# Kernel tuning notes

Measured on AMD Instinct MI355X. Metric: run time of the kernel, lower is better.

## Reference

```python
import jax, jax.numpy as jnp
import numpy as np

B, N, F, R, H = 128, 196, 2048, 1024, 512

def setup_inputs() -> dict:
    key = jax.random.key(0)
    ks = jax.random.split(key, 16)
    u = lambda k, shape, s=0.1: jax.random.uniform(k, shape, jnp.float32, -s, s)
    inp = {
        'att_seq': jax.random.normal(ks[0], (B, N, F), jnp.float32),
        'mil_feats': jax.random.normal(ks[1], (B, 1000), jnp.float32),
        'matching_feats': jax.random.normal(ks[2], (B, 1000), jnp.float32),
        'h': jax.random.normal(ks[3], (B, R), jnp.float32),
        'c': jax.random.normal(ks[4], (B, R), jnp.float32),
        # params (torch Linear convention: W [out,in], y = x@W.T + b)
        'W_att': u(ks[5], (H, F)), 'b_att': jnp.zeros((H,), jnp.float32),
        'W_hatt': u(ks[6], (H, R)), 'b_hatt': jnp.zeros((H,), jnp.float32),
        'w_out': u(ks[7], (1, H)), 'b_out': jnp.zeros((1,), jnp.float32),
        'W_h2h': u(ks[8], (4 * R, R)), 'b_h2h': jnp.full((4 * R,), -1.0, jnp.float32),
        'W_z2h': u(ks[9], (4 * R, F)), 'b_z2h': jnp.full((4 * R,), -1.0, jnp.float32),
    }
    return inp

def reference(att_seq, mil_feats, matching_feats, h, c,
              W_att, b_att, W_hatt, b_hatt, w_out, b_out,
              W_h2h, b_h2h, W_z2h, b_z2h):
    # additive (Bahdanau) attention scores
    att_linear = jnp.einsum('bnf,hf->bnh', att_seq, W_att) + b_att        # [B,N,H]
    h_linear = h @ W_hatt.T + b_hatt                                      # [B,H]
    att_h = jnp.tanh(att_linear + h_linear[:, None, :])                   # [B,N,H]
    scores = jnp.einsum('bnh,h->bn', att_h, w_out[0]) + b_out[0]          # [B,N]
    conv_weight = jax.nn.softmax(scores, axis=-1)                         # [B,N]
    z = jnp.einsum('bnf,bn->bf', att_seq, conv_weight)                    # [B,F]
    # LSTM step
    all_input_sums = h @ W_h2h.T + b_h2h + z @ W_z2h.T + b_z2h            # [B,4R]
    sig = jax.nn.sigmoid(all_input_sums[:, :3 * R])
    in_gate, forget_gate, out_gate = sig[:, :R], sig[:, R:2 * R], sig[:, 2 * R:3 * R]
    in_transform = jnp.tanh(all_input_sums[:, 3 * R:4 * R])
    next_c = forget_gate * c + in_gate * in_transform
    next_h = out_gate * jnp.tanh(next_c)
    return next_h, next_c
```

## Files before the change

kernel.cpp:

```cpp
#include <hip/hip_runtime.h>
#include <hip/hip_bf16.h>
#include <cstdint>
#include <cstddef>

#define Bb   128
#define Nn   196
#define Ff   2048
#define Rr   1024
#define Hh   512
#define Mm   (Bb*Nn)
#define KT   32

using short8   = __attribute__((ext_vector_type(8))) short;
using ushort8v = __attribute__((ext_vector_type(8))) unsigned short;
using f32x4    = __attribute__((ext_vector_type(4))) float;

typedef const __attribute__((address_space(1))) void cas1_void;
typedef __attribute__((address_space(3))) void as3_void;

static __device__ __forceinline__ unsigned short f2bf(float f) {
    unsigned int u = __float_as_uint(f);
    unsigned int r = (u + 0x7FFFu + ((u >> 16) & 1u)) >> 16;
    return (unsigned short)r;
}
static __device__ __forceinline__ float bf2f(unsigned short s) {
    return __uint_as_float(((unsigned int)s) << 16);
}
static __device__ __forceinline__ float sigmf(float x) {
    return 1.0f / (1.0f + expf(-x));
}

__global__ void cvt_watt_kernel(const float* __restrict__ W, unsigned short* __restrict__ wbt) {
    int g = blockIdx.x * 256 + threadIdx.x;
    int n = g >> 8;
    int k = (g & 255) * 8;
    float4 v0 = *reinterpret_cast<const float4*>(&W[(size_t)n * Ff + k]);
    float4 v1 = *reinterpret_cast<const float4*>(&W[(size_t)n * Ff + k + 4]);
    ushort8v u;
    u[0]=f2bf(v0.x); u[1]=f2bf(v0.y); u[2]=f2bf(v0.z); u[3]=f2bf(v0.w);
    u[4]=f2bf(v1.x); u[5]=f2bf(v1.y); u[6]=f2bf(v1.z); u[7]=f2bf(v1.w);
    int nb = n >> 7, row = n & 127, kb = k >> 6, c = (k >> 3) & 7;
    *reinterpret_cast<ushort8v*>(
        &wbt[((size_t)nb * KT + kb) * 8192 + row * 64 + ((c ^ (row & 7)) * 8)]) = u;
}

__global__ __launch_bounds__(512) void cvt_att_kernel(
    const float* __restrict__ att, unsigned short* __restrict__ attbf) {
    const int bm = blockIdx.x, t = threadIdx.x;
    const int cl = t & 15;
    const int rb = t >> 4;
    unsigned short* obase = attbf + (size_t)bm * (KT * 8192);
#pragma unroll
    for (int p = 0; p < 4; ++p) {
        int r = p * 32 + rb;
        const float* src = att + (size_t)(bm * 128 + r) * Ff + cl * 128;
        unsigned short* orow = obase + r * 64;
        int swz = r & 7;
#pragma unroll
        for (int jj = 0; jj < 16; ++jj) {
            float4 v0 = *reinterpret_cast<const float4*>(src + jj * 8);
            float4 v1 = *reinterpret_cast<const float4*>(src + jj * 8 + 4);
            ushort8v u;
            u[0]=f2bf(v0.x); u[1]=f2bf(v0.y); u[2]=f2bf(v0.z); u[3]=f2bf(v0.w);
            u[4]=f2bf(v1.x); u[5]=f2bf(v1.y); u[6]=f2bf(v1.z); u[7]=f2bf(v1.w);
            int k = cl * 128 + jj * 8;
            int kb = k >> 6, c = (k >> 3) & 7;
            *reinterpret_cast<ushort8v*>(&orow[kb * 8192 + ((c ^ swz) * 8)]) = u;
        }
    }
}

__global__ __launch_bounds__(512) void hb_kernel(
    const float* __restrict__ h, const float* __restrict__ W_hatt,
    const float* __restrict__ b_att, const float* __restrict__ b_hatt,
    float* __restrict__ hb) {
    __shared__ float hs[Rr];
    const int b = blockIdx.x, t = threadIdx.x;
    *reinterpret_cast<float2*>(&hs[t * 2]) =
        *reinterpret_cast<const float2*>(&h[(size_t)b * Rr + t * 2]);
    __syncthreads();
    const float* wr = &W_hatt[(size_t)t * Rr];
    float acc = 0.f;
#pragma unroll 4
    for (int k = 0; k < Rr; k += 4) {
        float4 w4 = *reinterpret_cast<const float4*>(&wr[k]);
        acc += w4.x * hs[k] + w4.y * hs[k + 1] + w4.z * hs[k + 2] + w4.w * hs[k + 3];
    }
    hb[(size_t)b * Hh + t] = acc + b_att[t] + b_hatt[t];
}

__global__ __launch_bounds__(256, 3) void gemmB_kernel(
    const unsigned short* __restrict__ attbf, const unsigned short* __restrict__ wbt,
    const float* __restrict__ hb, const float* __restrict__ w_out,
    float* __restrict__ scores_part) {
    __shared__ __align__(16) unsigned short Asub[8192];
    __shared__ __align__(16) unsigned short Bsub[8192];
    __shared__ float s_red[128];

    const int t = threadIdx.x;
    const int bm = blockIdx.x;
    const int bn = blockIdx.y;
    const int m0 = bm * 128;
    const int wave = t >> 6, lane = t & 63;
    const int l15 = lane & 15, lhi = lane >> 4;
    const int wm = wave >> 1, wn = wave & 1;

    if (t < 128) s_red[t] = 0.f;

    f32x4 acc[4][4] = {};

    const char* abase = (const char*)(attbf + (size_t)bm * (KT * 8192));
    const char* bbase = (const char*)(wbt   + (size_t)bn * (KT * 8192));
    const int off = wave * 1024 + lane * 16;

    for (int kt = 0; kt < KT; ++kt) {
        __syncthreads();
        const char* ab = abase + kt * 16384;
        const char* bb = bbase + kt * 16384;
#pragma unroll
        for (int i = 0; i < 4; ++i) {
            __builtin_amdgcn_global_load_lds(
                (cas1_void*)(ab + i * 4096 + off),
                (as3_void*)((char*)Asub + i * 4096 + wave * 1024), 16, 0, 0);
            __builtin_amdgcn_global_load_lds(
                (cas1_void*)(bb + i * 4096 + off),
                (as3_void*)((char*)Bsub + i * 4096 + wave * 1024), 16, 0, 0);
        }
        __syncthreads();
#pragma unroll
        for (int kk = 0; kk < 2; ++kk) {
            short8 a[4], b[4];
#pragma unroll
            for (int mi = 0; mi < 4; ++mi) {
                int row = wm * 64 + mi * 16 + l15;
                int ch = (kk * 4 + lhi) ^ (row & 7);
                a[mi] = *reinterpret_cast<const short8*>(&Asub[row * 64 + ch * 8]);
            }
#pragma unroll
            for (int ni = 0; ni < 4; ++ni) {
                int row = wn * 64 + ni * 16 + l15;
                int ch = (kk * 4 + lhi) ^ (row & 7);
                b[ni] = *reinterpret_cast<const short8*>(&Bsub[row * 64 + ch * 8]);
            }
#pragma unroll
            for (int mi = 0; mi < 4; ++mi)
#pragma unroll
                for (int ni = 0; ni < 4; ++ni)
                    acc[mi][ni] = __builtin_amdgcn_mfma_f32_16x16x32_bf16(
                        a[mi], b[ni], acc[mi][ni], 0, 0, 0);
        }
    }

#pragma unroll
    for (int mi = 0; mi < 4; ++mi) {
#pragma unroll
        for (int r = 0; r < 4; ++r) {
            int m_local = wm * 64 + mi * 16 + lhi * 4 + r;
            int m = m0 + m_local;
            int bidx = m / Nn;
            float sum = 0.f;
#pragma unroll
            for (int ni = 0; ni < 4; ++ni) {
                int n = bn * 128 + wn * 64 + ni * 16 + l15;
                float v = acc[mi][ni][r] + hb[(size_t)bidx * Hh + n];
                sum += tanhf(v) * w_out[n];
            }
            sum += __shfl_xor(sum, 1);
            sum += __shfl_xor(sum, 2);
            sum += __shfl_xor(sum, 4);
            sum += __shfl_xor(sum, 8);
            if (l15 == 0) atomicAdd(&s_red[m_local], sum);
        }
    }
    __syncthreads();
    if (t < 128) scores_part[(size_t)blockIdx.y * Mm + m0 + t] = s_red[t];
}

__global__ void softmax_kernel(const float* __restrict__ sp, float* __restrict__ conv) {
    __shared__ float redm[4];
    __shared__ float reds[4];
    const int b = blockIdx.x, t = threadIdx.x;
    float s = -1e30f;
    if (t < Nn) {
        size_t i = (size_t)b * Nn + t;
        s = sp[i] + sp[Mm + i] + sp[2 * (size_t)Mm + i] + sp[3 * (size_t)Mm + i];
    }
    float v = s;
#pragma unroll
    for (int o = 1; o < 64; o <<= 1) v = fmaxf(v, __shfl_xor(v, o));
    if ((t & 63) == 0) redm[t >> 6] = v;
    __syncthreads();
    float mx = fmaxf(fmaxf(redm[0], redm[1]), fmaxf(redm[2], redm[3]));
    float e = (t < Nn) ? expf(s - mx) : 0.f;
    float sv = e;
#pragma unroll
    for (int o = 1; o < 64; o <<= 1) sv += __shfl_xor(sv, o);
    if ((t & 63) == 0) reds[t >> 6] = sv;
    __syncthreads();
    float tot = reds[0] + reds[1] + reds[2] + reds[3];
    if (t < Nn) conv[(size_t)b * Nn + t] = e / tot;
}

__global__ __launch_bounds__(256) void zpart_kernel(
    const float* __restrict__ att, const float* __restrict__ conv,
    float* __restrict__ zp) {
    const int fc = blockIdx.x;
    const int b  = blockIdx.y;
    const int ns = blockIdx.z;
    const int t  = threadIdx.x;
    const int f  = fc * 1024 + t * 4;
    const int nbeg = ns * 28;
    const float* ab = &att[((size_t)b * Nn + nbeg) * Ff + f];
    const float* cw = &conv[(size_t)b * Nn + nbeg];
    float4 acc = {0.f, 0.f, 0.f, 0.f};
#pragma unroll 7
    for (int n = 0; n < 28; ++n) {
        float w = cw[n];
        float4 a = *reinterpret_cast<const float4*>(&ab[(size_t)n * Ff]);
        acc.x += w * a.x; acc.y += w * a.y; acc.z += w * a.z; acc.w += w * a.w;
    }
    *reinterpret_cast<float4*>(&zp[((size_t)ns * Bb + b) * Ff + f]) = acc;
}

__global__ void zcomb_kernel(const float* __restrict__ zp, float* __restrict__ z) {
    const size_t i = ((size_t)blockIdx.x * 256 + threadIdx.x) * 4;
    float4 o = {0.f, 0.f, 0.f, 0.f};
#pragma unroll
    for (int s = 0; s < 7; ++s) {
        float4 a = *reinterpret_cast<const float4*>(&zp[(size_t)s * 262144 + i]);
        o.x += a.x; o.y += a.y; o.z += a.z; o.w += a.w;
    }
    *reinterpret_cast<float4*>(&z[i]) = o;
}

__global__ void cvt_hz_kernel(const float* __restrict__ h, const float* __restrict__ z,
                              unsigned short* __restrict__ hzh, unsigned short* __restrict__ hzl) {
    int i = blockIdx.x * 256 + threadIdx.x;
    int e = i * 4;
    int row = e / 3072, col = e - row * 3072;
    const float* src = (col < 1024) ? &h[(size_t)row * Rr + col]
                                    : &z[(size_t)row * Ff + (col - 1024)];
    float4 v = *reinterpret_cast<const float4*>(src);
    ushort4 uh, ul;
    uh.x = f2bf(v.x); ul.x = f2bf(v.x - bf2f(uh.x));
    uh.y = f2bf(v.y); ul.y = f2bf(v.y - bf2f(uh.y));
    uh.z = f2bf(v.z); ul.z = f2bf(v.z - bf2f(uh.z));
    uh.w = f2bf(v.w); ul.w = f2bf(v.w - bf2f(uh.w));
    *reinterpret_cast<ushort4*>(&hzh[e]) = uh;
    *reinterpret_cast<ushort4*>(&hzl[e]) = ul;
}

__global__ __launch_bounds__(256, 2) void gemm2_kernel(
    const unsigned short* __restrict__ hzh, const unsigned short* __restrict__ hzl,
    const float* __restrict__ Wh2h, const float* __restrict__ Wz2h,
    float* __restrict__ Sp) {
    __shared__ __align__(16) unsigned short Ah[128][72];
    __shared__ __align__(16) unsigned short Al[128][72];
    __shared__ __align__(16) unsigned short Bh[32][72];
    __shared__ __align__(16) unsigned short Bl[32][72];

    const int t = threadIdx.x;
    const int n0 = blockIdx.x * 32;
    const int kc = blockIdx.y;
    const int kbeg = kc * 768;
    const int wave = t >> 6, lane = t & 63;
    const int l15 = lane & 15, lhi = lane >> 4;
    const int wm = wave >> 1, wn = wave & 1;

    f32x4 acc[4] = {};

    for (int k0 = kbeg; k0 < kbeg + 768; k0 += 64) {
        __syncthreads();
#pragma unroll
        for (int i = 0; i < 4; ++i) {
            int idx = i * 256 + t;
            int row = idx >> 3, k8 = idx & 7;
            *reinterpret_cast<int4*>(&Ah[row][k8 * 8]) =
                *reinterpret_cast<const int4*>(&hzh[(size_t)row * 3072 + k0 + k8 * 8]);
            *reinterpret_cast<int4*>(&Al[row][k8 * 8]) =
                *reinterpret_cast<const int4*>(&hzl[(size_t)row * 3072 + k0 + k8 * 8]);
        }
        const bool hpart = (k0 < 1024);
#pragma unroll
        for (int i = 0; i < 2; ++i) {
            int idx = i * 256 + t;
            int row = idx >> 4, kq = idx & 15;
            int kg = k0 + kq * 4;
            int n = n0 + row;
            const float* src = hpart ? &Wh2h[(size_t)n * Rr + kg]
                                     : &Wz2h[(size_t)n * Ff + (kg - 1024)];
            float4 v = *reinterpret_cast<const float4*>(src);
            ushort4 uh, ul;
            uh.x = f2bf(v.x); ul.x = f2bf(v.x - bf2f(uh.x));
            uh.y = f2bf(v.y); ul.y = f2bf(v.y - bf2f(uh.y));
            uh.z = f2bf(v.z); ul.z = f2bf(v.z - bf2f(uh.z));
            uh.w = f2bf(v.w); ul.w = f2bf(v.w - bf2f(uh.w));
            *reinterpret_cast<ushort4*>(&Bh[row][kq * 4]) = uh;
            *reinterpret_cast<ushort4*>(&Bl[row][kq * 4]) = ul;
        }
        __syncthreads();
#pragma unroll
        for (int kk = 0; kk < 2; ++kk) {
            short8 bhf = *reinterpret_cast<const short8*>(
                &Bh[wn * 16 + l15][kk * 32 + lhi * 8]);
            short8 blf = *reinterpret_cast<const short8*>(
                &Bl[wn * 16 + l15][kk * 32 + lhi * 8]);
#pragma unroll
            for (int mi = 0; mi < 4; ++mi) {
                short8 ahf = *reinterpret_cast<const short8*>(
                    &Ah[wm * 64 + mi * 16 + l15][kk * 32 + lhi * 8]);
                short8 alf = *reinterpret_cast<const short8*>(
                    &Al[wm * 64 + mi * 16 + l15][kk * 32 + lhi * 8]);
                acc[mi] = __builtin_amdgcn_mfma_f32_16x16x32_bf16(ahf, bhf, acc[mi], 0, 0, 0);
                acc[mi] = __builtin_amdgcn_mfma_f32_16x16x32_bf16(ahf, blf, acc[mi], 0, 0, 0);
                acc[mi] = __builtin_amdgcn_mfma_f32_16x16x32_bf16(alf, bhf, acc[mi], 0, 0, 0);
            }
        }
    }
    const int n = n0 + wn * 16 + l15;
#pragma unroll
    for (int mi = 0; mi < 4; ++mi)
#pragma unroll
        for (int r = 0; r < 4; ++r) {
            int brow = wm * 64 + mi * 16 + lhi * 4 + r;
            Sp[(((size_t)kc * Bb) + brow) * 4096 + n] = acc[mi][r];
        }
}

__global__ void lstm_kernel(const float* __restrict__ Sp, const float* __restrict__ c,
                            const float* __restrict__ bh2h, const float* __restrict__ bz2h,
                            float* __restrict__ out) {
    const int t = blockIdx.x * 256 + threadIdx.x;
    const int b = t >> 10, r = t & 1023;
    float s0 = 0.f, s1 = 0.f, s2 = 0.f, s3 = 0.f;
#pragma unroll
    for (int kc = 0; kc < 4; ++kc) {
        const float* Sb = &Sp[((size_t)kc * Bb + b) * 4096];
        s0 += Sb[r]; s1 += Sb[1024 + r]; s2 += Sb[2048 + r]; s3 += Sb[3072 + r];
    }
    float ig = sigmf(s0 + bh2h[r] + bz2h[r]);
    float fg = sigmf(s1 + bh2h[1024 + r] + bz2h[1024 + r]);
    float og = sigmf(s2 + bh2h[2048 + r] + bz2h[2048 + r]);
    float gt = tanhf(s3 + bh2h[3072 + r] + bz2h[3072 + r]);
    float nc = fg * c[t] + ig * gt;
    float nh = og * tanhf(nc);
    out[t] = nh;
    out[131072 + t] = nc;
}

extern "C" void kernel_launch(void* const* d_in, const int* in_sizes, int n_in,
                              void* d_out, int out_size, void* d_ws, size_t ws_size,
                              hipStream_t stream) {
    const float* att     = (const float*)d_in[0];
    const float* h       = (const float*)d_in[3];
    const float* c       = (const float*)d_in[4];
    const float* W_att   = (const float*)d_in[5];
    const float* b_att   = (const float*)d_in[6];
    const float* W_hatt  = (const float*)d_in[7];
    const float* b_hatt  = (const float*)d_in[8];
    const float* w_out   = (const float*)d_in[9];
    const float* W_h2h   = (const float*)d_in[11];
    const float* b_h2h   = (const float*)d_in[12];
    const float* W_z2h   = (const float*)d_in[13];
    const float* b_z2h   = (const float*)d_in[14];
    float* out = (float*)d_out;

    char* ws = (char*)d_ws;
    size_t o = 0;
    unsigned short* attbf = (unsigned short*)(ws + o); o += (size_t)196 * KT * 8192 * 2;
    unsigned short* wbt   = (unsigned short*)(ws + o); o += (size_t)4 * KT * 8192 * 2;
    float* hb             = (float*)(ws + o);          o += (size_t)Bb * Hh * 4;
    float* sp             = (float*)(ws + o);          o += (size_t)4 * Mm * 4;
    float* conv           = (float*)(ws + o);          o += (size_t)Bb * Nn * 4 + 256;
    float* zp             = (float*)(ws + o);          o += (size_t)7 * Bb * Ff * 4;
    float* z              = (float*)(ws + o);          o += (size_t)Bb * Ff * 4;
    float* Sp             = (float*)(ws + o);          o += (size_t)4 * Bb * 4096 * 4;
    unsigned short* hzh   = (unsigned short*)(ws + o); o += (size_t)Bb * 3072 * 2;
    unsigned short* hzl   = (unsigned short*)(ws + o); o += (size_t)Bb * 3072 * 2;

    cvt_watt_kernel<<<512, 256, 0, stream>>>(W_att, wbt);
    cvt_att_kernel<<<196, 512, 0, stream>>>(att, attbf);
    hb_kernel<<<Bb, 512, 0, stream>>>(h, W_hatt, b_att, b_hatt, hb);
    gemmB_kernel<<<dim3(196, 4), 256, 0, stream>>>(attbf, wbt, hb, w_out, sp);
    softmax_kernel<<<Bb, 256, 0, stream>>>(sp, conv);
    zpart_kernel<<<dim3(2, Bb, 7), 256, 0, stream>>>(att, conv, zp);
    zcomb_kernel<<<256, 256, 0, stream>>>(zp, z);
    cvt_hz_kernel<<<384, 256, 0, stream>>>(h, z, hzh, hzl);
    gemm2_kernel<<<dim3(128, 4), 256, 0, stream>>>(hzh, hzl, W_h2h, W_z2h, Sp);
    lstm_kernel<<<512, 256, 0, stream>>>(Sp, c, b_h2h, b_z2h, out);
}
```

Measured before the change: 647.1 us.

## Read bf16 attention copy in z reduction and retile conversion and GEMM grid

The z weighted sum now reads the bf16 swizzled copy of att_seq instead of the fp32 original, halving that pass's memory traffic. The att conversion kernel is retiled so each block writes one contiguous 128x64 tile with coalesced stores and many more blocks. The attention GEMM grid is transposed so the four N-blocks sharing an A tile run adjacently, improving L2 reuse of A. Using bf16 att in z adds rounding error to the LSTM inputs.

New measurement: 551.6 us. 14.8% less time.

```diff
diff --git a/kernel.cpp b/kernel.cpp
--- a/kernel.cpp
+++ b/kernel.cpp
@@ -44,29 +44,25 @@
         &wbt[((size_t)nb * KT + kb) * 8192 + row * 64 + ((c ^ (row & 7)) * 8)]) = u;
 }
 
-__global__ __launch_bounds__(512) void cvt_att_kernel(
+__global__ __launch_bounds__(256) void cvt_att_kernel(
     const float* __restrict__ att, unsigned short* __restrict__ attbf) {
-    const int bm = blockIdx.x, t = threadIdx.x;
-    const int cl = t & 15;
-    const int rb = t >> 4;
-    unsigned short* obase = attbf + (size_t)bm * (KT * 8192);
-#pragma unroll
-    for (int p = 0; p < 4; ++p) {
-        int r = p * 32 + rb;
-        const float* src = att + (size_t)(bm * 128 + r) * Ff + cl * 128;
-        unsigned short* orow = obase + r * 64;
-        int swz = r & 7;
-#pragma unroll
-        for (int jj = 0; jj < 16; ++jj) {
-            float4 v0 = *reinterpret_cast<const float4*>(src + jj * 8);
-            float4 v1 = *reinterpret_cast<const float4*>(src + jj * 8 + 4);
-            ushort8v u;
-            u[0]=f2bf(v0.x); u[1]=f2bf(v0.y); u[2]=f2bf(v0.z); u[3]=f2bf(v0.w);
-            u[4]=f2bf(v1.x); u[5]=f2bf(v1.y); u[6]=f2bf(v1.z); u[7]=f2bf(v1.w);
-            int k = cl * 128 + jj * 8;
-            int kb = k >> 6, c = (k >> 3) & 7;
-            *reinterpret_cast<ushort8v*>(&orow[kb * 8192 + ((c ^ swz) * 8)]) = u;
-        }
+    const int tile = blockIdx.x;
+    const int bm = tile >> 5, kb = tile & 31;
+    const int t = threadIdx.x;
+    unsigned short* out = attbf + (size_t)tile * 8192;
+    const float* abase = att + (size_t)bm * 128 * Ff + kb * 64;
+#pragma unroll
+    for (int it = 0; it < 4; ++it) {
+        int idx = it * 256 + t;
+        int row = idx >> 3, p = idx & 7;
+        int k = (p ^ (row & 7)) * 8;
+        const float* src = abase + (size_t)row * Ff + k;
+        float4 v0 = *reinterpret_cast<const float4*>(src);
+        float4 v1 = *reinterpret_cast<const float4*>(src + 4);
+        ushort8v u;
+        u[0]=f2bf(v0.x); u[1]=f2bf(v0.y); u[2]=f2bf(v0.z); u[3]=f2bf(v0.w);
+        u[4]=f2bf(v1.x); u[5]=f2bf(v1.y); u[6]=f2bf(v1.z); u[7]=f2bf(v1.w);
+        *reinterpret_cast<ushort8v*>(out + idx * 8) = u;
     }
 }
 
@@ -98,8 +94,8 @@
     __shared__ float s_red[128];
 
     const int t = threadIdx.x;
-    const int bm = blockIdx.x;
-    const int bn = blockIdx.y;
+    const int bn = blockIdx.x;
+    const int bm = blockIdx.y;
     const int m0 = bm * 128;
     const int wave = t >> 6, lane = t & 63;
     const int l15 = lane & 15, lhi = lane >> 4;
@@ -173,7 +169,7 @@
         }
     }
     __syncthreads();
-    if (t < 128) scores_part[(size_t)blockIdx.y * Mm + m0 + t] = s_red[t];
+    if (t < 128) scores_part[(size_t)bn * Mm + m0 + t] = s_red[t];
 }
 
 __global__ void softmax_kernel(const float* __restrict__ sp, float* __restrict__ conv) {
@@ -202,24 +198,30 @@
 }
 
 __global__ __launch_bounds__(256) void zpart_kernel(
-    const float* __restrict__ att, const float* __restrict__ conv,
+    const unsigned short* __restrict__ attbf, const float* __restrict__ conv,
     float* __restrict__ zp) {
-    const int fc = blockIdx.x;
-    const int b  = blockIdx.y;
-    const int ns = blockIdx.z;
+    const int b  = blockIdx.x;
+    const int ns = blockIdx.y;
     const int t  = threadIdx.x;
-    const int f  = fc * 1024 + t * 4;
+    const int kb = t >> 3, c = t & 7;
     const int nbeg = ns * 28;
-    const float* ab = &att[((size_t)b * Nn + nbeg) * Ff + f];
     const float* cw = &conv[(size_t)b * Nn + nbeg];
-    float4 acc = {0.f, 0.f, 0.f, 0.f};
-#pragma unroll 7
+    float acc[8] = {};
     for (int n = 0; n < 28; ++n) {
+        int m = b * Nn + nbeg + n;
+        int bm = m >> 7, row = m & 127;
+        const unsigned short* src =
+            attbf + ((size_t)(bm * KT + kb)) * 8192 + row * 64 + ((c ^ (row & 7)) * 8);
+        ushort8v u = *reinterpret_cast<const ushort8v*>(src);
         float w = cw[n];
-        float4 a = *reinterpret_cast<const float4*>(&ab[(size_t)n * Ff]);
-        acc.x += w * a.x; acc.y += w * a.y; acc.z += w * a.z; acc.w += w * a.w;
-    }
-    *reinterpret_cast<float4*>(&zp[((size_t)ns * Bb + b) * Ff + f]) = acc;
+#pragma unroll
+        for (int j = 0; j < 8; ++j) acc[j] += w * bf2f(u[j]);
+    }
+    float4 o0 = {acc[0], acc[1], acc[2], acc[3]};
+    float4 o1 = {acc[4], acc[5], acc[6], acc[7]};
+    float* dst = &zp[((size_t)ns * Bb + b) * Ff + t * 8];
+    *reinterpret_cast<float4*>(dst) = o0;
+    *reinterpret_cast<float4*>(dst + 4) = o1;
 }
 
 __global__ void zcomb_kernel(const float* __restrict__ zp, float* __restrict__ z) {
@@ -379,11 +381,11 @@
     unsigned short* hzl   = (unsigned short*)(ws + o); o += (size_t)Bb * 3072 * 2;
 
     cvt_watt_kernel<<<512, 256, 0, stream>>>(W_att, wbt);
-    cvt_att_kernel<<<196, 512, 0, stream>>>(att, attbf);
+    cvt_att_kernel<<<196 * KT, 256, 0, stream>>>(att, attbf);
     hb_kernel<<<Bb, 512, 0, stream>>>(h, W_hatt, b_att, b_hatt, hb);
-    gemmB_kernel<<<dim3(196, 4), 256, 0, stream>>>(attbf, wbt, hb, w_out, sp);
+    gemmB_kernel<<<dim3(4, 196), 256, 0, stream>>>(attbf, wbt, hb, w_out, sp);
     softmax_kernel<<<Bb, 256, 0, stream>>>(sp, conv);
-    zpart_kernel<<<dim3(2, Bb, 7), 256, 0, stream>>>(att, conv, zp);
+    zpart_kernel<<<dim3(Bb, 7), 256, 0, stream>>>(attbf, conv, zp);
     zcomb_kernel<<<256, 256, 0, stream>>>(zp, z);
     cvt_hz_kernel<<<384, 256, 0, stream>>>(h, z, hzh, hzl);
     gemm2_kernel<<<dim3(128, 4), 256, 0, stream>>>(hzh, hzl, W_h2h, W_z2h, Sp);
```
